# Performance work log

Hardware: AMD Instinct MI355X
Metric: run time of the kernel (lower is better)

The kernel has to match this reference:

```python
import jax, jax.numpy as jnp
import numpy as np

GN_GROUPS = 32
GN_EPS = 1e-6


def setup_inputs() -> dict:
    key = jax.random.key(0)
    ks = jax.random.split(key, 4)
    B, C, H, W = 8, 512, 32, 32
    x = jax.random.normal(ks[0], (B, C, H, W), dtype=jnp.float32)
    W_qkv = jax.random.normal(ks[1], (C, 3 * C), dtype=jnp.float32) * 0.02
    b_qkv = jnp.zeros((3 * C,), dtype=jnp.float32)
    W_out = jax.random.normal(ks[2], (C, C), dtype=jnp.float32) * 0.02
    b_out = jnp.zeros((C,), dtype=jnp.float32)
    gn_scale = jnp.ones((C,), dtype=jnp.float32)
    gn_bias = jnp.zeros((C,), dtype=jnp.float32)
    return {"x": x, "gn_scale": gn_scale, "gn_bias": gn_bias,
            "W_qkv": W_qkv, "b_qkv": b_qkv, "W_out": W_out, "b_out": b_out,
            "num_heads": 8}


def _group_norm(x, scale, bias):
    B, C, H, W = x.shape
    g = GN_GROUPS
    xg = x.reshape(B, g, C // g, H * W)
    mean = xg.mean(axis=(2, 3), keepdims=True)
    var = xg.var(axis=(2, 3), keepdims=True)
    xg = (xg - mean) * jax.lax.rsqrt(var + GN_EPS)
    x = xg.reshape(B, C, H, W)
    return x * scale[None, :, None, None] + bias[None, :, None, None]


def reference(x, gn_scale, gn_bias, W_qkv, b_qkv, W_out, b_out, num_heads):
    B, C, H, W = x.shape
    hd = C // num_heads
    h = _group_norm(x, gn_scale, gn_bias)
    # NIN: 1x1 projection over channels -> (B, 3C, H, W)
    h = jnp.einsum('bchw,cd->bdhw', h, W_qkv) + b_qkv[None, :, None, None]
    # reshape exactly like torch: (B, nh, 3*hd, HW) then move seq last->middle
    h = h.reshape(B, num_heads, 3 * hd, H * W).transpose(0, 1, 3, 2)  # (B, nh, S, 3hd)
    q, k, v = jnp.split(h, 3, axis=-1)  # each (B, nh, S, hd)
    scale = 1.0 / jnp.sqrt(jnp.asarray(hd, dtype=q.dtype))
    logits = jnp.einsum('bhsd,bhtd->bhst', q, k) * scale  # (B, nh, S, S)
    attn = jax.nn.softmax(logits, axis=-1)
    vals = jnp.einsum('bhst,bhtd->bhsd', attn, v)  # (B, nh, S, hd)
    h = vals.transpose(0, 1, 3, 2).reshape(B, C, H, W)
    h = jnp.einsum('bchw,cd->bdhw', h, W_out) + b_out[None, :, None, None]
    return x + h
```

## Files before the change

### kernel.cpp

```cpp
#include <hip/hip_runtime.h>
#include <hip/hip_bf16.h>

typedef __bf16 bf16_t;
typedef __attribute__((ext_vector_type(8))) __bf16 bf16x8;
typedef __attribute__((ext_vector_type(4))) float f32x4;
typedef __attribute__((ext_vector_type(4))) unsigned int u32x4;

#define B_   8
#define C_   512
#define S_   1024
#define NH   8
#define C2_  1024
#define C3_  1536
#define QSCALE 0.1803368801111204f

static __device__ __forceinline__ unsigned pack2(float a, float b) {
  unsigned short lo = __builtin_bit_cast(unsigned short, (bf16_t)a);
  unsigned short hi = __builtin_bit_cast(unsigned short, (bf16_t)b);
  return (unsigned)lo | ((unsigned)hi << 16);
}

static __device__ __forceinline__ void load_lds16(const void* g, void* l) {
  __builtin_amdgcn_global_load_lds(
      (const __attribute__((address_space(1))) unsigned*)g,
      (__attribute__((address_space(3))) unsigned*)l, 16, 0, 0);
}

template<int ROUNDS>
static __device__ __forceinline__ void stage_swz(const bf16_t* g, int rstride,
                                                 char* lbuf, int tid) {
#pragma unroll
  for (int r = 0; r < ROUNDS; ++r) {
    int i = r * 256 + tid;
    int row = i >> 3;
    int cg = (i & 7) ^ (row & 7);
    load_lds16(g + (size_t)row * rstride + cg * 8,
               lbuf + r * 4096 + (tid & 192) * 16);
  }
}

static __device__ __forceinline__ void stage_swz512(const bf16_t* g, int rstride,
                                                    char* lbuf, int tid) {
  int row = tid >> 3;
  int cg = (tid & 7) ^ (row & 7);
  load_lds16(g + (size_t)row * rstride + cg * 8,
             lbuf + (tid & 448) * 16);
}

__global__ __launch_bounds__(256) void gn_kernel(
    const float* __restrict__ x, const float* __restrict__ scale,
    const float* __restrict__ bias, bf16_t* __restrict__ h_t) {
  __shared__ float xs[16 * 1024];
  __shared__ float red[8];
  int b = blockIdx.x >> 5, g = blockIdx.x & 31;
  int tid = threadIdx.x;
  const f32x4* xb4 = (const f32x4*)(x + ((size_t)b * C_ + g * 16) * S_);

  float s = 0.f, s2 = 0.f;
#pragma unroll
  for (int k = 0; k < 16; ++k) {
    int vf = k * 256 + tid;
    f32x4 v = xb4[vf];
    ((f32x4*)xs)[vf] = v;
#pragma unroll
    for (int e = 0; e < 4; ++e) { s += v[e]; s2 += v[e] * v[e]; }
  }
  for (int off = 32; off > 0; off >>= 1) {
    s  += __shfl_down(s, off);
    s2 += __shfl_down(s2, off);
  }
  int wave = tid >> 6, lane = tid & 63;
  if (lane == 0) { red[wave] = s; red[4 + wave] = s2; }
  __syncthreads();
  float ts = red[0] + red[1] + red[2] + red[3];
  float t2 = red[4] + red[5] + red[6] + red[7];
  const float inv_n = 1.f / (16.f * S_);
  float mean = ts * inv_n;
  float var  = t2 * inv_n - mean * mean;
  float rstd = rsqrtf(var + 1e-6f);

  float ac[16], bc[16];
#pragma unroll
  for (int cl = 0; cl < 16; ++cl) {
    float sc = scale[g * 16 + cl] * rstd;
    ac[cl] = sc;
    bc[cl] = bias[g * 16 + cl] - mean * sc;
  }
#pragma unroll
  for (int k = 0; k < 4; ++k) {
    int srow = tid + k * 256;
    unsigned ow[8];
#pragma unroll
    for (int p = 0; p < 8; ++p) {
      float y0 = xs[(2 * p    ) * 1024 + srow] * ac[2 * p    ] + bc[2 * p    ];
      float y1 = xs[(2 * p + 1) * 1024 + srow] * ac[2 * p + 1] + bc[2 * p + 1];
      ow[p] = pack2(y0, y1);
    }
    bf16_t* dst = h_t + ((size_t)b * S_ + srow) * C_ + g * 16;
    u32x4 v0, v1;
#pragma unroll
    for (int e = 0; e < 4; ++e) { v0[e] = ow[e]; v1[e] = ow[4 + e]; }
    *(u32x4*)dst = v0;
    *(u32x4*)(dst + 8) = v1;
  }
}

__global__ __launch_bounds__(256) void prep_wqkv_kernel(
    const float* __restrict__ W, const float* __restrict__ bq,
    bf16_t* __restrict__ Wt, float* __restrict__ bt) {
  __shared__ float T[32 * 33];
  int d0 = blockIdx.x * 32, c0 = blockIdx.y * 32;
  int tid = threadIdx.x, ld = tid & 31, lc = tid >> 5;
#pragma unroll
  for (int i = 0; i < 4; ++i) {
    int c = lc + i * 8;
    T[c * 33 + ld] = W[(size_t)(c0 + c) * C3_ + d0 + ld];
  }
  __syncthreads();
#pragma unroll
  for (int i = 0; i < 4; ++i) {
    int dd = lc + i * 8;
    int d = d0 + dd;
    int h = d / 192, rr = d - h * 192, part = rr >> 6, dq = rr & 63;
    float scl = (part == 0) ? QSCALE : 1.f;
    Wt[(size_t)(part * 512 + h * 64 + dq) * C_ + c0 + ld] =
        (bf16_t)(T[ld * 33 + dd] * scl);
  }
  if (blockIdx.y == 0 && tid < 32) {
    int d = d0 + tid;
    int h = d / 192, rr = d - h * 192, part = rr >> 6, dq = rr & 63;
    bt[part * 512 + h * 64 + dq] = bq[d] * ((part == 0) ? QSCALE : 1.f);
  }
}

__global__ __launch_bounds__(256) void transpose_w_kernel(
    const float* __restrict__ W, bf16_t* __restrict__ Wt, int R, int Ccols) {
  __shared__ float T[32 * 33];
  int c0 = blockIdx.x * 32, r0 = blockIdx.y * 32;
  int tid = threadIdx.x;
  int lc = tid & 31, lr = tid >> 5;
  for (int i = 0; i < 4; ++i) {
    int r = lr + i * 8;
    T[r * 33 + lc] = W[(size_t)(r0 + r) * Ccols + c0 + lc];
  }
  __syncthreads();
  for (int i = 0; i < 4; ++i) {
    int cc = lr + i * 8;
    Wt[(size_t)(c0 + cc) * R + r0 + lc] = (bf16_t)T[lc * 33 + cc];
  }
}

template<int MF, int NF>
static __device__ __forceinline__ void gemm_loop(
    const bf16_t* Asrc, int Astride, const bf16_t* Bsrc, int Bstride,
    char* lds, int tid, f32x4 (&acc)[MF][NF]) {
  int wave = tid >> 6, lane = tid & 63;
  int wr = wave >> 1, wc = wave & 1;
  int lr = lane & 15, lq = lane >> 4;
  char* A0 = lds;
  char* B0 = lds + MF * 4096;
  char* A1 = lds + (MF + NF) * 4096;
  char* B1 = lds + (2 * MF + NF) * 4096;
  stage_swz<MF>(Asrc, Astride, A0, tid);
  stage_swz<NF>(Bsrc, Bstride, B0, tid);
#pragma unroll 1
  for (int ks = 0; ks < 8; ++ks) {
    if (ks < 7) {
      stage_swz<MF>(Asrc + (ks + 1) * 64, Astride, (ks & 1) ? A0 : A1, tid);
      stage_swz<NF>(Bsrc + (ks + 1) * 64, Bstride, (ks & 1) ? B0 : B1, tid);
      asm volatile("s_waitcnt vmcnt(%0)" :: "i"(MF + NF) : "memory");
    } else {
      asm volatile("s_waitcnt vmcnt(0)" ::: "memory");
    }
    __builtin_amdgcn_s_barrier();
    const char* Ab = (ks & 1) ? A1 : A0;
    const char* Bb = (ks & 1) ? B1 : B0;
#pragma unroll
    for (int kk = 0; kk < 2; ++kk) {
      int co = ((kk * 4 + lq) ^ (lr & 7)) << 4;
      bf16x8 a[MF], b[NF];
#pragma unroll
      for (int i = 0; i < MF; ++i)
        a[i] = *(const bf16x8*)(Ab + (wr * MF * 16 + i * 16 + lr) * 128 + co);
#pragma unroll
      for (int j = 0; j < NF; ++j)
        b[j] = *(const bf16x8*)(Bb + (wc * NF * 16 + j * 16 + lr) * 128 + co);
#pragma unroll
      for (int i = 0; i < MF; ++i)
#pragma unroll
        for (int j = 0; j < NF; ++j)
          acc[i][j] = __builtin_amdgcn_mfma_f32_16x16x32_bf16(a[i], b[j], acc[i][j], 0, 0, 0);
    }
    __builtin_amdgcn_s_barrier();
  }
}

__global__ __launch_bounds__(256) void gemm_qkv_kernel(
    const bf16_t* __restrict__ h, const bf16_t* __restrict__ wq,
    const float* __restrict__ bias, bf16_t* __restrict__ qk,
    bf16_t* __restrict__ vt) {
  __shared__ char lds[65536];
  int tid = threadIdx.x;
  int bid = blockIdx.x;
  int wave = tid >> 6, lane = tid & 63;
  int wr = wave >> 1, wc = wave & 1, lr = lane & 15, lq = lane >> 4;
  unsigned short* tb = (unsigned short*)lds;
  if (bid < 512) {
    int m0 = (bid & 63) * 128, n0 = (bid >> 6) * 128;
    f32x4 acc[4][4] = {};
    gemm_loop<4, 4>(h + (size_t)m0 * C_, C_, wq + (size_t)n0 * C_, C_, lds, tid, acc);
    float bv[4];
#pragma unroll
    for (int j = 0; j < 4; ++j) bv[j] = bias[n0 + wc * 64 + j * 16 + lr];
#pragma unroll
    for (int i = 0; i < 4; ++i)
#pragma unroll
      for (int j = 0; j < 4; ++j)
#pragma unroll
        for (int r = 0; r < 4; ++r) {
          int row = wr * 64 + i * 16 + lq * 4 + r;
          int col = wc * 64 + j * 16 + lr;
          int byte = row * 256 + (((col >> 3) ^ (row & 7)) << 4) + ((col & 7) << 1);
          tb[byte >> 1] = __builtin_bit_cast(unsigned short, (bf16_t)(acc[i][j][r] + bv[j]));
        }
    __builtin_amdgcn_s_barrier();
#pragma unroll
    for (int u = 0; u < 8; ++u) {
      int flat = tid + u * 256;
      int row = flat >> 4, c = flat & 15;
      u32x4 v = *(const u32x4*)(lds + row * 256 + ((c ^ (row & 7)) << 4));
      int m = m0 + row, b = m >> 10, s = m & 1023;
      int d = n0 + c * 8;
      int hh = (d >> 6) & 7, det = ((d >> 9) << 6) + (d & 63);
      *(u32x4*)(qk + ((size_t)(b * S_ + s)) * C2_ + hh * 128 + det) = v;
    }
  } else {
    int j2 = bid - 512;
    int n0 = (j2 & 63) * 128, m0 = (j2 >> 6) * 128;
    f32x4 acc[4][4] = {};
    gemm_loop<4, 4>(wq + (size_t)(1024 + m0) * C_, C_, h + (size_t)n0 * C_, C_, lds, tid, acc);
    float bv[4][4];
#pragma unroll
    for (int i = 0; i < 4; ++i) {
      f32x4 t = *(const f32x4*)(bias + 1024 + m0 + wr * 64 + i * 16 + lq * 4);
#pragma unroll
      for (int r = 0; r < 4; ++r) bv[i][r] = t[r];
    }
#pragma unroll
    for (int i = 0; i < 4; ++i)
#pragma unroll
      for (int j = 0; j < 4; ++j)
#pragma unroll
        for (int r = 0; r < 4; ++r) {
          int row = wr * 64 + i * 16 + lq * 4 + r;
          int col = wc * 64 + j * 16 + lr;
          int byte = row * 256 + (((col >> 3) ^ (row & 7)) << 4) + ((col & 7) << 1);
          tb[byte >> 1] = __builtin_bit_cast(unsigned short, (bf16_t)(acc[i][j][r] + bv[i][r]));
        }
    __builtin_amdgcn_s_barrier();
#pragma unroll
    for (int u = 0; u < 8; ++u) {
      int flat = tid + u * 256;
      int row = flat >> 4, c = flat & 15;
      u32x4 v = *(const u32x4*)(lds + row * 256 + ((c ^ (row & 7)) << 4));
      int m = m0 + row;
      int hh = m >> 6, dv = m & 63;
      int n = n0 + c * 8, b = n >> 10, s = n & 1023;
      *(u32x4*)(vt + ((size_t)((b * NH + hh) * 64 + dv)) * S_ + s) = v;
    }
  }
}

__global__ __launch_bounds__(512) void attn_kernel(
    const bf16_t* __restrict__ qk, const bf16_t* __restrict__ vt,
    bf16_t* __restrict__ ao) {
  __shared__ char lds[49152];
  int bid = blockIdx.x;
  int qt = bid >> 6, g = bid & 63;
  int b = g >> 3, head = g & 7;
  int tid = threadIdx.x, wave = tid >> 6, lane = tid & 63;
  int lr = lane & 15, lq = lane >> 4;
  int qb = qt * 128 + wave * 16;
  const bf16_t* qkb = qk + (size_t)b * S_ * C2_ + head * 128;
  const bf16_t* vtb = vt + (size_t)((b * NH + head) * 64) * S_;

  bf16x8 qf[2];
#pragma unroll
  for (int kk = 0; kk < 2; ++kk)
    qf[kk] = *(const bf16x8*)(qkb + (size_t)(qb + lr) * C2_ + kk * 32 + lq * 8);

  f32x4 oacc[4] = {};
  float m_run = -1e30f, l_run = 0.f;

  char* sb0 = lds;
  char* sb1 = lds + 16384;
  char* sb2 = lds + 32768;

#define STAGE_KV(kt, buf)                                                    \
  do {                                                                       \
    stage_swz512(qkb + (size_t)((kt) * 64) * C2_ + 64, C2_, (buf), tid);     \
    stage_swz512(vtb + (kt) * 64, S_, (buf) + 8192, tid);                    \
  } while (0)

  STAGE_KV(0, sb0);
#pragma unroll 1
  for (int kt = 0; kt < 16; ++kt) {
    if (kt < 15) {
      STAGE_KV(kt + 1, sb1);
      asm volatile("s_waitcnt vmcnt(2)" ::: "memory");
    } else {
      asm volatile("s_waitcnt vmcnt(0)" ::: "memory");
    }
    __builtin_amdgcn_s_barrier();

    f32x4 sacc[4] = {};
    __builtin_amdgcn_s_setprio(1);
#pragma unroll
    for (int kk = 0; kk < 2; ++kk) {
      int co = ((kk * 4 + lq) ^ (lr & 7)) << 4;
#pragma unroll
      for (int mf = 0; mf < 4; ++mf) {
        bf16x8 kf = *(const bf16x8*)(sb0 + (mf * 16 + lr) * 128 + co);
        sacc[mf] = __builtin_amdgcn_mfma_f32_16x16x32_bf16(kf, qf[kk], sacc[mf], 0, 0, 0);
      }
    }
    __builtin_amdgcn_s_setprio(0);

    float mx = -1e30f;
#pragma unroll
    for (int mf = 0; mf < 4; ++mf)
#pragma unroll
      for (int r = 0; r < 4; ++r) mx = fmaxf(mx, sacc[mf][r]);
    mx = fmaxf(mx, __shfl_xor(mx, 16));
    mx = fmaxf(mx, __shfl_xor(mx, 32));
    if (__any(mx - m_run > 11.f)) {
      float mn = fmaxf(m_run, mx);
      float alpha = __builtin_amdgcn_exp2f(m_run - mn);
      m_run = mn;
      l_run *= alpha;
#pragma unroll
      for (int df = 0; df < 4; ++df)
#pragma unroll
        for (int r = 0; r < 4; ++r) oacc[df][r] *= alpha;
    }
    float p[4][4];
    float rs = 0.f;
#pragma unroll
    for (int mf = 0; mf < 4; ++mf)
#pragma unroll
      for (int r = 0; r < 4; ++r) {
        float v = __builtin_amdgcn_exp2f(sacc[mf][r] - m_run);
        p[mf][r] = v; rs += v;
      }
    l_run += rs;
    unsigned pk[4][2];
#pragma unroll
    for (int mf = 0; mf < 4; ++mf)
#pragma unroll
      for (int j = 0; j < 2; ++j)
        pk[mf][j] = pack2(p[mf][2 * j], p[mf][2 * j + 1]);

#pragma unroll
    for (int kk = 0; kk < 2; ++kk) {
      int co = ((kk * 4 + lq) ^ (lr & 7)) << 4;
      bf16x8 vf[4];
#pragma unroll
      for (int df = 0; df < 4; ++df)
        vf[df] = *(const bf16x8*)(sb0 + 8192 + (df * 16 + lr) * 128 + co);
      unsigned w0 = pk[2 * kk + 0][0], w2 = pk[2 * kk + 1][0];
      unsigned w1 = pk[2 * kk + 0][1], w3 = pk[2 * kk + 1][1];
      asm("v_permlane32_swap_b32 %0, %1" : "+v"(w0), "+v"(w2));
      asm("v_permlane16_swap_b32 %0, %1" : "+v"(w0), "+v"(w2));
      asm("v_permlane32_swap_b32 %0, %1" : "+v"(w1), "+v"(w3));
      asm("v_permlane16_swap_b32 %0, %1" : "+v"(w1), "+v"(w3));
      u32x4 bw; bw[0] = w0; bw[1] = w1; bw[2] = w2; bw[3] = w3;
      bf16x8 pb = __builtin_bit_cast(bf16x8, bw);
      __builtin_amdgcn_s_setprio(1);
#pragma unroll
      for (int df = 0; df < 4; ++df)
        oacc[df] = __builtin_amdgcn_mfma_f32_16x16x32_bf16(vf[df], pb, oacc[df], 0, 0, 0);
      __builtin_amdgcn_s_setprio(0);
    }
    char* tp = sb0; sb0 = sb1; sb1 = sb2; sb2 = tp;
  }

  float lt = l_run;
  lt += __shfl_xor(lt, 16);
  lt += __shfl_xor(lt, 32);
  float inv = 1.f / lt;
  bf16_t* aop = ao + ((size_t)b * S_ + qb + lr) * C_ + head * 64;
#pragma unroll
  for (int df = 0; df < 4; ++df)
#pragma unroll
    for (int rp = 0; rp < 4; rp += 2) {
      unsigned u = pack2(oacc[df][rp] * inv, oacc[df][rp + 1] * inv);
      *(unsigned*)(aop + df * 16 + lq * 4 + rp) = u;
    }
#undef STAGE_KV
}

__global__ __launch_bounds__(256) void gemm_out_kernel(
    const bf16_t* __restrict__ A, const bf16_t* __restrict__ Bw,
    const float* __restrict__ bias, const float* __restrict__ xres,
    float* __restrict__ out) {
  __shared__ char lds[49152];
  int tid = threadIdx.x;
  int bid = blockIdx.x;
  int m0 = (bid & 127) * 64, n0 = (bid >> 7) * 128;
  f32x4 acc[2][4] = {};
  gemm_loop<2, 4>(A + (size_t)m0 * C_, C_, Bw + (size_t)n0 * C_, C_, lds, tid, acc);
  int wave = tid >> 6, lane = tid & 63;
  int wr = wave >> 1, wc = wave & 1, lr = lane & 15, lq = lane >> 4;
#pragma unroll
  for (int i = 0; i < 2; ++i) {
#pragma unroll
    for (int j = 0; j < 4; ++j) {
      int d = n0 + wc * 64 + j * 16 + lr;
      int m = m0 + wr * 32 + i * 16 + lq * 4;
      int b = m >> 10, s = m & 1023;
      size_t o = ((size_t)b * C_ + d) * S_ + s;
      f32x4 res = *(const f32x4*)(xres + o);
      f32x4 val;
      float bd = bias[d];
#pragma unroll
      for (int r = 0; r < 4; ++r) val[r] = res[r] + bd + acc[i][j][r];
      *(f32x4*)(out + o) = val;
    }
  }
}

extern "C" void kernel_launch(void* const* d_in, const int* in_sizes, int n_in,
                              void* d_out, int out_size, void* d_ws, size_t ws_size,
                              hipStream_t stream) {
  const float* x        = (const float*)d_in[0];
  const float* gn_scale = (const float*)d_in[1];
  const float* gn_bias  = (const float*)d_in[2];
  const float* W_qkv    = (const float*)d_in[3];
  const float* b_qkv    = (const float*)d_in[4];
  const float* W_out    = (const float*)d_in[5];
  const float* b_out    = (const float*)d_in[6];
  float* out = (float*)d_out;

  char* ws = (char*)d_ws;
  bf16_t* h_t   = (bf16_t*)(ws);
  bf16_t* qk_t  = (bf16_t*)(ws + 8388608);
  bf16_t* vt    = (bf16_t*)(ws + 25165824);
  bf16_t* ao_t  = (bf16_t*)(ws + 33554432);
  bf16_t* wqkvp = (bf16_t*)(ws + 41943040);
  bf16_t* woutt = (bf16_t*)(ws + 43515904);
  float* bqp = (float*)d_out;

  prep_wqkv_kernel<<<dim3(48, 16), 256, 0, stream>>>(W_qkv, b_qkv, wqkvp, bqp);
  transpose_w_kernel<<<dim3(16, 16), 256, 0, stream>>>(W_out, woutt, C_, C_);
  gn_kernel<<<256, 256, 0, stream>>>(x, gn_scale, gn_bias, h_t);
  gemm_qkv_kernel<<<768, 256, 0, stream>>>(h_t, wqkvp, bqp, qk_t, vt);
  attn_kernel<<<512, 512, 0, stream>>>(qk_t, vt, ao_t);
  gemm_out_kernel<<<512, 256, 0, stream>>>(ao_t, woutt, b_out, x, out);
}
```

Measured before the change: 82.22 us.

## Merge prep kernels into one launch; attention processes two query tiles per wave

Folds the three preprocessing kernels (GroupNorm, QKV weight permute, out-weight transpose) into one launch using block-index dispatch, removing two launch gaps. The attention kernel now has each wave handle 32 query rows, two 16-row fragments. Each K/V fragment read from LDS is reused for both, and the KV prefetch ring deepens to four buffers with two tiles in flight. This halves the attention grid to 256 blocks, which may underfill the GPU's CUs, and raises register pressure and LDS use to 64KB. The merged prep kernel also gives every block the 64KB GroupNorm shared-memory allocation, which can limit occupancy for the weight-transpose blocks.

```diff
diff --git a/kernel.cpp b/kernel.cpp
--- a/kernel.cpp
+++ b/kernel.cpp
@@ -47,106 +47,107 @@
              lbuf + (tid & 448) * 16);
 }
 
-__global__ __launch_bounds__(256) void gn_kernel(
-    const float* __restrict__ x, const float* __restrict__ scale,
-    const float* __restrict__ bias, bf16_t* __restrict__ h_t) {
-  __shared__ float xs[16 * 1024];
-  __shared__ float red[8];
-  int b = blockIdx.x >> 5, g = blockIdx.x & 31;
+__global__ __launch_bounds__(256) void prep_kernel(
+    const float* __restrict__ x, const float* __restrict__ gsc,
+    const float* __restrict__ gbi, const float* __restrict__ Wq,
+    const float* __restrict__ bq, const float* __restrict__ Wo,
+    bf16_t* __restrict__ h_t, bf16_t* __restrict__ wqkvp,
+    bf16_t* __restrict__ woutt, float* __restrict__ bqp) {
+  __shared__ __align__(16) char smem[65568];
+  int bid = blockIdx.x;
   int tid = threadIdx.x;
-  const f32x4* xb4 = (const f32x4*)(x + ((size_t)b * C_ + g * 16) * S_);
-
-  float s = 0.f, s2 = 0.f;
-#pragma unroll
-  for (int k = 0; k < 16; ++k) {
-    int vf = k * 256 + tid;
-    f32x4 v = xb4[vf];
-    ((f32x4*)xs)[vf] = v;
-#pragma unroll
-    for (int e = 0; e < 4; ++e) { s += v[e]; s2 += v[e] * v[e]; }
-  }
-  for (int off = 32; off > 0; off >>= 1) {
-    s  += __shfl_down(s, off);
-    s2 += __shfl_down(s2, off);
-  }
-  int wave = tid >> 6, lane = tid & 63;
-  if (lane == 0) { red[wave] = s; red[4 + wave] = s2; }
-  __syncthreads();
-  float ts = red[0] + red[1] + red[2] + red[3];
-  float t2 = red[4] + red[5] + red[6] + red[7];
-  const float inv_n = 1.f / (16.f * S_);
-  float mean = ts * inv_n;
-  float var  = t2 * inv_n - mean * mean;
-  float rstd = rsqrtf(var + 1e-6f);
-
-  float ac[16], bc[16];
-#pragma unroll
-  for (int cl = 0; cl < 16; ++cl) {
-    float sc = scale[g * 16 + cl] * rstd;
-    ac[cl] = sc;
-    bc[cl] = bias[g * 16 + cl] - mean * sc;
-  }
-#pragma unroll
-  for (int k = 0; k < 4; ++k) {
-    int srow = tid + k * 256;
-    unsigned ow[8];
-#pragma unroll
-    for (int p = 0; p < 8; ++p) {
-      float y0 = xs[(2 * p    ) * 1024 + srow] * ac[2 * p    ] + bc[2 * p    ];
-      float y1 = xs[(2 * p + 1) * 1024 + srow] * ac[2 * p + 1] + bc[2 * p + 1];
-      ow[p] = pack2(y0, y1);
-    }
-    bf16_t* dst = h_t + ((size_t)b * S_ + srow) * C_ + g * 16;
-    u32x4 v0, v1;
-#pragma unroll
-    for (int e = 0; e < 4; ++e) { v0[e] = ow[e]; v1[e] = ow[4 + e]; }
-    *(u32x4*)dst = v0;
-    *(u32x4*)(dst + 8) = v1;
-  }
-}
-
-__global__ __launch_bounds__(256) void prep_wqkv_kernel(
-    const float* __restrict__ W, const float* __restrict__ bq,
-    bf16_t* __restrict__ Wt, float* __restrict__ bt) {
-  __shared__ float T[32 * 33];
-  int d0 = blockIdx.x * 32, c0 = blockIdx.y * 32;
-  int tid = threadIdx.x, ld = tid & 31, lc = tid >> 5;
-#pragma unroll
-  for (int i = 0; i < 4; ++i) {
-    int c = lc + i * 8;
-    T[c * 33 + ld] = W[(size_t)(c0 + c) * C3_ + d0 + ld];
-  }
-  __syncthreads();
-#pragma unroll
-  for (int i = 0; i < 4; ++i) {
-    int dd = lc + i * 8;
-    int d = d0 + dd;
-    int h = d / 192, rr = d - h * 192, part = rr >> 6, dq = rr & 63;
-    float scl = (part == 0) ? QSCALE : 1.f;
-    Wt[(size_t)(part * 512 + h * 64 + dq) * C_ + c0 + ld] =
-        (bf16_t)(T[ld * 33 + dd] * scl);
-  }
-  if (blockIdx.y == 0 && tid < 32) {
-    int d = d0 + tid;
-    int h = d / 192, rr = d - h * 192, part = rr >> 6, dq = rr & 63;
-    bt[part * 512 + h * 64 + dq] = bq[d] * ((part == 0) ? QSCALE : 1.f);
-  }
-}
-
-__global__ __launch_bounds__(256) void transpose_w_kernel(
-    const float* __restrict__ W, bf16_t* __restrict__ Wt, int R, int Ccols) {
-  __shared__ float T[32 * 33];
-  int c0 = blockIdx.x * 32, r0 = blockIdx.y * 32;
-  int tid = threadIdx.x;
-  int lc = tid & 31, lr = tid >> 5;
-  for (int i = 0; i < 4; ++i) {
-    int r = lr + i * 8;
-    T[r * 33 + lc] = W[(size_t)(r0 + r) * Ccols + c0 + lc];
-  }
-  __syncthreads();
-  for (int i = 0; i < 4; ++i) {
-    int cc = lr + i * 8;
-    Wt[(size_t)(c0 + cc) * R + r0 + lc] = (bf16_t)T[lc * 33 + cc];
+  if (bid < 256) {
+    float* xs = (float*)smem;
+    float* red = (float*)(smem + 65536);
+    int b = bid >> 5, g = bid & 31;
+    const f32x4* xb4 = (const f32x4*)(x + ((size_t)b * C_ + g * 16) * S_);
+    float s = 0.f, s2 = 0.f;
+#pragma unroll
+    for (int k = 0; k < 16; ++k) {
+      int vf = k * 256 + tid;
+      f32x4 v = xb4[vf];
+      ((f32x4*)xs)[vf] = v;
+#pragma unroll
+      for (int e = 0; e < 4; ++e) { s += v[e]; s2 += v[e] * v[e]; }
+    }
+    for (int off = 32; off > 0; off >>= 1) {
+      s  += __shfl_down(s, off);
+      s2 += __shfl_down(s2, off);
+    }
+    int wave = tid >> 6, lane = tid & 63;
+    if (lane == 0) { red[wave] = s; red[4 + wave] = s2; }
+    __syncthreads();
+    float ts = red[0] + red[1] + red[2] + red[3];
+    float t2 = red[4] + red[5] + red[6] + red[7];
+    const float inv_n = 1.f / (16.f * S_);
+    float mean = ts * inv_n;
+    float var  = t2 * inv_n - mean * mean;
+    float rstd = rsqrtf(var + 1e-6f);
+    float ac[16], bc[16];
+#pragma unroll
+    for (int cl = 0; cl < 16; ++cl) {
+      float sc = gsc[g * 16 + cl] * rstd;
+      ac[cl] = sc;
+      bc[cl] = gbi[g * 16 + cl] - mean * sc;
+    }
+#pragma unroll
+    for (int k = 0; k < 4; ++k) {
+      int srow = tid + k * 256;
+      unsigned ow[8];
+#pragma unroll
+      for (int p = 0; p < 8; ++p) {
+        float y0 = xs[(2 * p    ) * 1024 + srow] * ac[2 * p    ] + bc[2 * p    ];
+        float y1 = xs[(2 * p + 1) * 1024 + srow] * ac[2 * p + 1] + bc[2 * p + 1];
+        ow[p] = pack2(y0, y1);
+      }
+      bf16_t* dst = h_t + ((size_t)b * S_ + srow) * C_ + g * 16;
+      u32x4 v0, v1;
+#pragma unroll
+      for (int e = 0; e < 4; ++e) { v0[e] = ow[e]; v1[e] = ow[4 + e]; }
+      *(u32x4*)dst = v0;
+      *(u32x4*)(dst + 8) = v1;
+    }
+  } else if (bid < 1024) {
+    float* T = (float*)smem;
+    int id = bid - 256;
+    int d0 = (id % 48) * 32, c0 = (id / 48) * 32;
+    int ld = tid & 31, lc = tid >> 5;
+#pragma unroll
+    for (int i = 0; i < 4; ++i) {
+      int c = lc + i * 8;
+      T[c * 33 + ld] = Wq[(size_t)(c0 + c) * C3_ + d0 + ld];
+    }
+    __syncthreads();
+#pragma unroll
+    for (int i = 0; i < 4; ++i) {
+      int dd = lc + i * 8;
+      int d = d0 + dd;
+      int h = d / 192, rr = d - h * 192, part = rr >> 6, dq = rr & 63;
+      float scl = (part == 0) ? QSCALE : 1.f;
+      wqkvp[(size_t)(part * 512 + h * 64 + dq) * C_ + c0 + ld] =
+          (bf16_t)(T[ld * 33 + dd] * scl);
+    }
+    if (id < 48 && tid < 32) {
+      int d = d0 + tid;
+      int h = d / 192, rr = d - h * 192, part = rr >> 6, dq = rr & 63;
+      bqp[part * 512 + h * 64 + dq] = bq[d] * ((part == 0) ? QSCALE : 1.f);
+    }
+  } else {
+    float* T = (float*)smem;
+    int id = bid - 1024;
+    int c0 = (id & 15) * 32, r0 = (id >> 4) * 32;
+    int lc = tid & 31, lr = tid >> 5;
+#pragma unroll
+    for (int i = 0; i < 4; ++i) {
+      int r = lr + i * 8;
+      T[r * 33 + lc] = Wo[(size_t)(r0 + r) * C_ + c0 + lc];
+    }
+    __syncthreads();
+#pragma unroll
+    for (int i = 0; i < 4; ++i) {
+      int cc = lr + i * 8;
+      woutt[(size_t)(c0 + cc) * C_ + r0 + lc] = (bf16_t)T[lc * 33 + cc];
+    }
   }
 }
 
@@ -274,27 +275,30 @@
 __global__ __launch_bounds__(512) void attn_kernel(
     const bf16_t* __restrict__ qk, const bf16_t* __restrict__ vt,
     bf16_t* __restrict__ ao) {
-  __shared__ char lds[49152];
+  __shared__ char lds[65536];
   int bid = blockIdx.x;
   int qt = bid >> 6, g = bid & 63;
   int b = g >> 3, head = g & 7;
   int tid = threadIdx.x, wave = tid >> 6, lane = tid & 63;
   int lr = lane & 15, lq = lane >> 4;
-  int qb = qt * 128 + wave * 16;
+  int qb = qt * 256 + wave * 32;
   const bf16_t* qkb = qk + (size_t)b * S_ * C2_ + head * 128;
   const bf16_t* vtb = vt + (size_t)((b * NH + head) * 64) * S_;
 
-  bf16x8 qf[2];
-#pragma unroll
-  for (int kk = 0; kk < 2; ++kk)
-    qf[kk] = *(const bf16x8*)(qkb + (size_t)(qb + lr) * C2_ + kk * 32 + lq * 8);
-
-  f32x4 oacc[4] = {};
-  float m_run = -1e30f, l_run = 0.f;
-
-  char* sb0 = lds;
-  char* sb1 = lds + 16384;
-  char* sb2 = lds + 32768;
+  bf16x8 qf[2][2];
+#pragma unroll
+  for (int q2 = 0; q2 < 2; ++q2)
+#pragma unroll
+    for (int kk = 0; kk < 2; ++kk)
+      qf[q2][kk] = *(const bf16x8*)(qkb + (size_t)(qb + q2 * 16 + lr) * C2_ + kk * 32 + lq * 8);
+
+  f32x4 oacc[2][4] = {};
+  float m_run[2] = {-1e30f, -1e30f}, l_run[2] = {0.f, 0.f};
+
+  char* s0 = lds;
+  char* s1 = lds + 16384;
+  char* s2 = lds + 32768;
+  char* s3 = lds + 49152;
 
 #define STAGE_KV(kt, buf)                                                    \
   do {                                                                       \
@@ -302,63 +306,81 @@
     stage_swz512(vtb + (kt) * 64, S_, (buf) + 8192, tid);                    \
   } while (0)
 
-  STAGE_KV(0, sb0);
+  STAGE_KV(0, s0);
+  STAGE_KV(1, s1);
 #pragma unroll 1
   for (int kt = 0; kt < 16; ++kt) {
-    if (kt < 15) {
-      STAGE_KV(kt + 1, sb1);
+    if (kt < 14) {
+      STAGE_KV(kt + 2, s2);
+      asm volatile("s_waitcnt vmcnt(4)" ::: "memory");
+    } else if (kt == 14) {
       asm volatile("s_waitcnt vmcnt(2)" ::: "memory");
     } else {
       asm volatile("s_waitcnt vmcnt(0)" ::: "memory");
     }
     __builtin_amdgcn_s_barrier();
 
-    f32x4 sacc[4] = {};
+    f32x4 sacc[2][4] = {};
     __builtin_amdgcn_s_setprio(1);
 #pragma unroll
     for (int kk = 0; kk < 2; ++kk) {
       int co = ((kk * 4 + lq) ^ (lr & 7)) << 4;
-#pragma unroll
-      for (int mf = 0; mf < 4; ++mf) {
-        bf16x8 kf = *(const bf16x8*)(sb0 + (mf * 16 + lr) * 128 + co);
-        sacc[mf] = __builtin_amdgcn_mfma_f32_16x16x32_bf16(kf, qf[kk], sacc[mf], 0, 0, 0);
+      bf16x8 kf[4];
+#pragma unroll
+      for (int mf = 0; mf < 4; ++mf)
+        kf[mf] = *(const bf16x8*)(s0 + (mf * 16 + lr) * 128 + co);
+#pragma unroll
+      for (int q2 = 0; q2 < 2; ++q2)
+#pragma unroll
+        for (int mf = 0; mf < 4; ++mf)
+          sacc[q2][mf] = __builtin_amdgcn_mfma_f32_16x16x32_bf16(kf[mf], qf[q2][kk], sacc[q2][mf], 0, 0, 0);
+    }
+    __builtin_amdgcn_s_setprio(0);
+
+    float mx[2];
+#pragma unroll
+    for (int q2 = 0; q2 < 2; ++q2) {
+      float m = -1e30f;
+#pragma unroll
+      for (int mf = 0; mf < 4; ++mf)
+#pragma unroll
+        for (int r = 0; r < 4; ++r) m = fmaxf(m, sacc[q2][mf][r]);
+      m = fmaxf(m, __shfl_xor(m, 16));
+      m = fmaxf(m, __shfl_xor(m, 32));
+      mx[q2] = m;
+    }
+    if (__any(fmaxf(mx[0] - m_run[0], mx[1] - m_run[1]) > 11.f)) {
+#pragma unroll
+      for (int q2 = 0; q2 < 2; ++q2) {
+        float mn = fmaxf(m_run[q2], mx[q2]);
+        float alpha = __builtin_amdgcn_exp2f(m_run[q2] - mn);
+        m_run[q2] = mn;
+        l_run[q2] *= alpha;
+#pragma unroll
+        for (int df = 0; df < 4; ++df)
+#pragma unroll
+          for (int r = 0; r < 4; ++r) oacc[q2][df][r] *= alpha;
       }
     }
-    __builtin_amdgcn_s_setprio(0);
-
-    float mx = -1e30f;
-#pragma unroll
-    for (int mf = 0; mf < 4; ++mf)
-#pragma unroll
-      for (int r = 0; r < 4; ++r) mx = fmaxf(mx, sacc[mf][r]);
-    mx = fmaxf(mx, __shfl_xor(mx, 16));
-    mx = fmaxf(mx, __shfl_xor(mx, 32));
-    if (__any(mx - m_run > 11.f)) {
-      float mn = fmaxf(m_run, mx);
-      float alpha = __builtin_amdgcn_exp2f(m_run - mn);
-      m_run = mn;
-      l_run *= alpha;
-#pragma unroll
-      for (int df = 0; df < 4; ++df)
-#pragma unroll
-        for (int r = 0; r < 4; ++r) oacc[df][r] *= alpha;
-    }
-    float p[4][4];
-    float rs = 0.f;
-#pragma unroll
-    for (int mf = 0; mf < 4; ++mf)
-#pragma unroll
-      for (int r = 0; r < 4; ++r) {
-        float v = __builtin_amdgcn_exp2f(sacc[mf][r] - m_run);
-        p[mf][r] = v; rs += v;
-      }
-    l_run += rs;
-    unsigned pk[4][2];
-#pragma unroll
-    for (int mf = 0; mf < 4; ++mf)
-#pragma unroll
-      for (int j = 0; j < 2; ++j)
-        pk[mf][j] = pack2(p[mf][2 * j], p[mf][2 * j + 1]);
+    unsigned pk[2][4][2];
+#pragma unroll
+    for (int q2 = 0; q2 < 2; ++q2) {
+      float p[4][4];
+      float rs = 0.f;
+#pragma unroll
+      for (int mf = 0; mf < 4; ++mf)
+#pragma unroll
+        for (int r = 0; r < 4; ++r) {
+          float v = __builtin_amdgcn_exp2f(sacc[q2][mf][r] - m_run[q2]);
+          p[mf][r] = v; rs += v;
+        }
+      l_run[q2] += rs;
+#pragma unroll
+      for (int mf = 0; mf < 4; ++mf)
+#pragma unroll
+        for (int j = 0; j < 2; ++j)
+          pk[q2][mf][j] = pack2(p[mf][2 * j], p[mf][2 * j + 1]);
+    }
 
 #pragma unroll
     for (int kk = 0; kk < 2; ++kk) {
@@ -366,36 +388,42 @@
       bf16x8 vf[4];
 #pragma unroll
       for (int df = 0; df < 4; ++df)
-        vf[df] = *(const bf16x8*)(sb0 + 8192 + (df * 16 + lr) * 128 + co);
-      unsigned w0 = pk[2 * kk + 0][0], w2 = pk[2 * kk + 1][0];
-      unsigned w1 = pk[2 * kk + 0][1], w3 = pk[2 * kk + 1][1];
-      asm("v_permlane32_swap_b32 %0, %1" : "+v"(w0), "+v"(w2));
-      asm("v_permlane16_swap_b32 %0, %1" : "+v"(w0), "+v"(w2));
-      asm("v_permlane32_swap_b32 %0, %1" : "+v"(w1), "+v"(w3));
-      asm("v_permlane16_swap_b32 %0, %1" : "+v"(w1), "+v"(w3));
-      u32x4 bw; bw[0] = w0; bw[1] = w1; bw[2] = w2; bw[3] = w3;
-      bf16x8 pb = __builtin_bit_cast(bf16x8, bw);
-      __builtin_amdgcn_s_setprio(1);
-#pragma unroll
-      for (int df = 0; df < 4; ++df)
-        oacc[df] = __builtin_amdgcn_mfma_f32_16x16x32_bf16(vf[df], pb, oacc[df], 0, 0, 0);
-      __builtin_amdgcn_s_setprio(0);
-    }
-    char* tp = sb0; sb0 = sb1; sb1 = sb2; sb2 = tp;
-  }
-
-  float lt = l_run;
-  lt += __shfl_xor(lt, 16);
-  lt += __shfl_xor(lt, 32);
-  float inv = 1.f / lt;
-  bf16_t* aop = ao + ((size_t)b * S_ + qb + lr) * C_ + head * 64;
-#pragma unroll
-  for (int df = 0; df < 4; ++df)
-#pragma unroll
-    for (int rp = 0; rp < 4; rp += 2) {
-      unsigned u = pack2(oacc[df][rp] * inv, oacc[df][rp + 1] * inv);
-      *(unsigned*)(aop + df * 16 + lq * 4 + rp) = u;
-    }
+        vf[df] = *(const bf16x8*)(s0 + 8192 + (df * 16 + lr) * 128 + co);
+#pragma unroll
+      for (int q2 = 0; q2 < 2; ++q2) {
+        unsigned w0 = pk[q2][2 * kk + 0][0], w2 = pk[q2][2 * kk + 1][0];
+        unsigned w1 = pk[q2][2 * kk + 0][1], w3 = pk[q2][2 * kk + 1][1];
+        asm("v_permlane32_swap_b32 %0, %1" : "+v"(w0), "+v"(w2));
+        asm("v_permlane16_swap_b32 %0, %1" : "+v"(w0), "+v"(w2));
+        asm("v_permlane32_swap_b32 %0, %1" : "+v"(w1), "+v"(w3));
+        asm("v_permlane16_swap_b32 %0, %1" : "+v"(w1), "+v"(w3));
+        u32x4 bw; bw[0] = w0; bw[1] = w1; bw[2] = w2; bw[3] = w3;
+        bf16x8 pb = __builtin_bit_cast(bf16x8, bw);
+        __builtin_amdgcn_s_setprio(1);
+#pragma unroll
+        for (int df = 0; df < 4; ++df)
+          oacc[q2][df] = __builtin_amdgcn_mfma_f32_16x16x32_bf16(vf[df], pb, oacc[q2][df], 0, 0, 0);
+        __builtin_amdgcn_s_setprio(0);
+      }
+    }
+    char* tp = s0; s0 = s1; s1 = s2; s2 = s3; s3 = tp;
+  }
+
+#pragma unroll
+  for (int q2 = 0; q2 < 2; ++q2) {
+    float lt = l_run[q2];
+    lt += __shfl_xor(lt, 16);
+    lt += __shfl_xor(lt, 32);
+    float inv = 1.f / lt;
+    bf16_t* aop = ao + ((size_t)b * S_ + qb + q2 * 16 + lr) * C_ + head * 64;
+#pragma unroll
+    for (int df = 0; df < 4; ++df)
+#pragma unroll
+      for (int rp = 0; rp < 4; rp += 2) {
+        unsigned u = pack2(oacc[q2][df][rp] * inv, oacc[q2][df][rp + 1] * inv);
+        *(unsigned*)(aop + df * 16 + lq * 4 + rp) = u;
+      }
+  }
 #undef STAGE_KV
 }
 
@@ -450,10 +478,9 @@
   bf16_t* woutt = (bf16_t*)(ws + 43515904);
   float* bqp = (float*)d_out;
 
-  prep_wqkv_kernel<<<dim3(48, 16), 256, 0, stream>>>(W_qkv, b_qkv, wqkvp, bqp);
-  transpose_w_kernel<<<dim3(16, 16), 256, 0, stream>>>(W_out, woutt, C_, C_);
-  gn_kernel<<<256, 256, 0, stream>>>(x, gn_scale, gn_bias, h_t);
+  prep_kernel<<<1280, 256, 0, stream>>>(x, gn_scale, gn_bias, W_qkv, b_qkv,
+                                        W_out, h_t, wqkvp, woutt, bqp);
   gemm_qkv_kernel<<<768, 256, 0, stream>>>(h_t, wqkvp, bqp, qk_t, vt);
-  attn_kernel<<<512, 512, 0, stream>>>(qk_t, vt, ao_t);
+  attn_kernel<<<256, 512, 0, stream>>>(qk_t, vt, ao_t);
   gemm_out_kernel<<<512, 256, 0, stream>>>(ao_t, woutt, b_out, x, out);
 }
```

Result: faster. 75.79 us (median of 2 runs) (-7.8%).
